# Kernel optimization log

Hardware: AMD Instinct MI355X
Metric: run time of the kernel (lower is better)

## Reference

```python
import jax, jax.numpy as jnp
import numpy as np

IN_CHANNELS = 8
CHANNELS = 8
MASK_OUT_STRIDE = 4
N_IMGS, H, W = 2, 128, 192
N_INST = 256
WEIGHT_NUMS = [(IN_CHANNELS + 2) * CHANNELS, CHANNELS * CHANNELS, CHANNELS * 1]  # [80, 64, 8]
BIAS_NUMS = [CHANNELS, CHANNELS, 1]
NUM_GEN_PARAMS = sum(WEIGHT_NUMS) + sum(BIAS_NUMS)  # 169


def setup_inputs() -> dict:
    key = jax.random.key(0)
    k1, k2, k3, k4, k5 = jax.random.split(key, 5)
    mask_feats = jax.random.normal(k1, (N_IMGS, IN_CHANNELS, H, W), dtype=jnp.float32)
    mask_head_params = jax.random.normal(k2, (N_INST, NUM_GEN_PARAMS), dtype=jnp.float32) * 0.1
    # instance center locations in image coordinates (stride-8 map covers 1024x1536 px)
    instance_locations = jax.random.uniform(k3, (N_INST, 2), dtype=jnp.float32) * jnp.array([W * 8.0, H * 8.0])
    soi = jnp.array([64.0, 128.0, 256.0, 512.0, 1024.0], dtype=jnp.float32)
    im_inds = jax.random.randint(k4, (N_INST,), 0, N_IMGS, dtype=jnp.int32)
    fpn_levels = jax.random.randint(k5, (N_INST,), 0, 5, dtype=jnp.int32)
    return {
        "mask_feats": mask_feats,
        "mask_head_params": mask_head_params,
        "instance_locations": instance_locations,
        "soi": soi,
        "im_inds": im_inds,
        "fpn_levels": fpn_levels,
        "mask_feat_stride": 8,
    }


def compute_locations(h, w, stride):
    shifts_x = jnp.arange(w, dtype=jnp.float32) * stride + stride // 2
    shifts_y = jnp.arange(h, dtype=jnp.float32) * stride + stride // 2
    ys, xs = jnp.meshgrid(shifts_y, shifts_x, indexing="ij")
    return jnp.stack([xs.ravel(), ys.ravel()], axis=1)  # [H*W, 2] (x, y)


def _interp_axis(x, size_in, factor, axis):
    # align_corners=True resize from (size_in+1) samples to (size_in*factor+1):
    # src coordinate of output i is exactly i / factor.
    idx = jnp.arange(size_in * factor + 1)
    i0 = idx // factor
    frac = ((idx % factor).astype(x.dtype)) / factor
    a = jnp.take(x, i0, axis=axis)
    b = jnp.take(x, jnp.minimum(i0 + 1, size_in), axis=axis)
    shape = [1] * x.ndim
    shape[axis] = -1
    f = frac.reshape(shape)
    return a * (1 - f) + b * f


def aligned_bilinear(t, factor):
    # Faithful to AdelaiDet aligned_bilinear: replicate-pad (0,1,0,1), bilinear
    # align_corners=True to (h*f+1, w*f+1), replicate-pad (f//2, 0) top/left, crop.
    if factor == 1:
        return t
    n, c, h, w = t.shape
    t = jnp.pad(t, ((0, 0), (0, 0), (0, 1), (0, 1)), mode="edge")
    t = _interp_axis(t, h, factor, 2)
    t = _interp_axis(t, w, factor, 3)
    p = factor // 2
    t = jnp.pad(t, ((0, 0), (0, 0), (p, 0), (p, 0)), mode="edge")
    return t[:, :, : h * factor, : w * factor]


def reference(mask_feats, mask_head_params, instance_locations, soi, im_inds, fpn_levels, mask_feat_stride):
    n_inst = mask_head_params.shape[0]
    _, c_in, h, w = mask_feats.shape
    hw = h * w

    # relative coordinates, normalized by size-of-interest per FPN level
    locations = compute_locations(h, w, mask_feat_stride)  # [HW, 2]
    rel = instance_locations[:, None, :] - locations[None, :, :]  # [n, HW, 2]
    rel = jnp.transpose(rel, (0, 2, 1))  # [n, 2, HW]
    rel = rel / soi[fpn_levels][:, None, None]
    rel = rel.astype(mask_feats.dtype)

    feats = mask_feats[im_inds].reshape(n_inst, c_in, hw)  # [n, C, HW]
    x = jnp.concatenate([rel, feats], axis=1)  # [n, C+2, HW]

    # parse dynamic params
    splits = np.cumsum(WEIGHT_NUMS + BIAS_NUMS)[:-1]
    w0, w1, w2, b0, b1, b2 = jnp.split(mask_head_params, splits, axis=1)
    w0 = w0.reshape(n_inst, CHANNELS, c_in + 2)
    w1 = w1.reshape(n_inst, CHANNELS, CHANNELS)
    w2 = w2.reshape(n_inst, 1, CHANNELS)

    # grouped 1x1 conv stack == per-instance batched matmul + bias (+ReLU)
    x = jax.nn.relu(jnp.einsum("noi,nip->nop", w0, x) + b0[:, :, None])
    x = jax.nn.relu(jnp.einsum("noi,nip->nop", w1, x) + b1[:, :, None])
    x = jnp.einsum("noi,nip->nop", w2, x) + b2[:, :, None]  # [n, 1, HW]

    logits = x.reshape(n_inst, 1, h, w)
    factor = mask_feat_stride // MASK_OUT_STRIDE
    return aligned_bilinear(logits, factor)  # [n, 1, h*factor, w*factor]
```

## Files before the change

### kernel.cpp

```cpp
#include <hip/hip_runtime.h>


#define HI 128
#define WI 192
#define HW_ (HI * WI)
#define NP 169
#define NOUT_W 384
#define NOUT_H 256

typedef float v2f __attribute__((ext_vector_type(2)));

__device__ __forceinline__ v2f splat(float x) { v2f r; r.x = x; r.y = x; return r; }
__device__ __forceinline__ v2f vfma(v2f a, v2f b, v2f c) {
    return __builtin_elementwise_fma(a, b, c);
}
__device__ __forceinline__ v2f vrelu(v2f a) {
    return __builtin_elementwise_max(a, splat(0.0f));
}

__global__ __launch_bounds__(512, 4) void dynmask_kernel(
    const float* __restrict__ feats,
    const float* __restrict__ params,
    const float* __restrict__ locs,
    const float* __restrict__ soi,
    const int*   __restrict__ im_inds,
    const int*   __restrict__ lvls,
    float*       __restrict__ out)
{
    __shared__ __align__(16) float L[65 * WI];

    const int b  = blockIdx.x;
    const int n  = b >> 1;
    const int hh = b & 1;
    const int t  = threadIdx.x;
    const int R0 = hh ? 63 : 0;

    const int   im    = im_inds[n];
    const float s     = soi[lvls[n]];
    const float inv_s = 1.0f / s;
    const float ixv   = locs[2 * n + 0];
    const float iyv   = locs[2 * n + 1];
    const float* __restrict__ P = params + n * NP;
    const float* __restrict__ F = feats + im * (8 * HW_);

    const float step = 8.0f * inv_s;
    const float ax   = (ixv - 4.0f) * inv_s;
    const float ay   = (iyv - 4.0f) * inv_s;

    for (int idx = t; idx < 3120; idx += 512) {
        const int p   = R0 * WI + (idx << 2);
        const int py  = p / WI;
        const int px0 = p - py * WI;
        const float ry  = ay - (float)py * step;
        const float rx0 = ax - (float)px0 * step;
        v2f rxp[2];
        rxp[0].x = rx0;                rxp[0].y = rx0 - step;
        rxp[1].x = rx0 - 2.0f * step;  rxp[1].y = rx0 - 3.0f * step;

        v2f fv[8][2];
        #pragma unroll
        for (int k = 0; k < 8; ++k) {
            const float4 v = *reinterpret_cast<const float4*>(F + k * HW_ + p);
            fv[k][0].x = v.x; fv[k][0].y = v.y;
            fv[k][1].x = v.z; fv[k][1].y = v.w;
        }

        v2f h0[8][2];
        #pragma unroll
        for (int o = 0; o < 8; ++o) {
            const float base = fmaf(P[o * 10 + 1], ry, P[152 + o]);
            const v2f   bv   = splat(base);
            const v2f   wx   = splat(P[o * 10 + 0]);
            h0[o][0] = vfma(wx, rxp[0], bv);
            h0[o][1] = vfma(wx, rxp[1], bv);
            #pragma unroll
            for (int k = 0; k < 8; ++k) {
                const v2f w = splat(P[o * 10 + 2 + k]);
                h0[o][0] = vfma(w, fv[k][0], h0[o][0]);
                h0[o][1] = vfma(w, fv[k][1], h0[o][1]);
            }
            h0[o][0] = vrelu(h0[o][0]);
            h0[o][1] = vrelu(h0[o][1]);
        }

        v2f h1[8][2];
        #pragma unroll
        for (int o = 0; o < 8; ++o) {
            const v2f bb = splat(P[160 + o]);
            h1[o][0] = bb;
            h1[o][1] = bb;
            #pragma unroll
            for (int i = 0; i < 8; ++i) {
                const v2f w = splat(P[80 + o * 8 + i]);
                h1[o][0] = vfma(w, h0[i][0], h1[o][0]);
                h1[o][1] = vfma(w, h0[i][1], h1[o][1]);
            }
            h1[o][0] = vrelu(h1[o][0]);
            h1[o][1] = vrelu(h1[o][1]);
        }

        v2f lg[2];
        lg[0] = splat(P[168]);
        lg[1] = lg[0];
        #pragma unroll
        for (int i = 0; i < 8; ++i) {
            const v2f w = splat(P[144 + i]);
            lg[0] = vfma(w, h1[i][0], lg[0]);
            lg[1] = vfma(w, h1[i][1], lg[1]);
        }

        float4 st;
        st.x = lg[0].x; st.y = lg[0].y; st.z = lg[1].x; st.w = lg[1].y;
        *reinterpret_cast<float4*>(&L[idx << 2]) = st;
    }

    __syncthreads();

    const int Y0 = hh << 7;
    float* __restrict__ O = out + n * (NOUT_H * NOUT_W) + Y0 * NOUT_W;
    for (int g = t; g < 6144; g += 512) {
        const int yq = g / 48;
        const int c  = g - yq * 48;
        const int y  = Y0 + yq;
        const int iy2 = (y == 0) ? 0 : (y - 1);
        const int ry0 = iy2 >> 1;
        const int fy  = iy2 & 1;
        const int lr0 = ry0 - R0;
        const int j0  = c << 2;
        const int jm  = (c == 0) ? 0 : (j0 - 1);

        const float* row0 = &L[lr0 * WI];
        float4 v  = *reinterpret_cast<const float4*>(row0 + j0);
        float  vm = row0[jm];
        if (fy) {
            const int lr1 = min(ry0 + 1, 127) - R0;
            const float* row1 = &L[lr1 * WI];
            const float4 w  = *reinterpret_cast<const float4*>(row1 + j0);
            const float  wm = row1[jm];
            v.x = 0.5f * (v.x + w.x); v.y = 0.5f * (v.y + w.y);
            v.z = 0.5f * (v.z + w.z); v.w = 0.5f * (v.w + w.w);
            vm  = 0.5f * (vm + wm);
        }
        float4 r0, r1;
        r0.x = 0.5f * (vm + v.x);  r0.y = v.x;
        r0.z = 0.5f * (v.x + v.y); r0.w = v.y;
        r1.x = 0.5f * (v.y + v.z); r1.y = v.z;
        r1.z = 0.5f * (v.z + v.w); r1.w = v.w;

        float* o8 = O + (g << 3);
        *reinterpret_cast<float4*>(o8)     = r0;
        *reinterpret_cast<float4*>(o8 + 4) = r1;
    }
}

extern "C" void kernel_launch(void* const* d_in, const int* in_sizes, int n_in,
                              void* d_out, int out_size, void* d_ws, size_t ws_size,
                              hipStream_t stream) {
    const float* feats   = (const float*)d_in[0];
    const float* params  = (const float*)d_in[1];
    const float* locs    = (const float*)d_in[2];
    const float* soi     = (const float*)d_in[3];
    const int*   im_inds = (const int*)d_in[4];
    const int*   lvls    = (const int*)d_in[5];
    float*       out     = (float*)d_out;
    dynmask_kernel<<<512, 512, 0, stream>>>(feats, params, locs, soi, im_inds, lvls, out);
}
```

Baseline: 149.9 us.

## Split each instance into four row quarters and halve per-thread pixel work

Each instance is now handled by four blocks covering 32 (+1 halo) logit rows instead of two blocks of 64, which doubles the grid and halves the shared-memory tile. Each thread computes 2 pixels instead of 4 with 8-byte loads, and launch bounds now request 8 blocks per CU, aiming for lower register pressure and higher occupancy. The trade-off is more redundant halo-row MLP work, narrower global loads, and more per-block parameter loads.

```diff
diff --git a/kernel.cpp b/kernel.cpp
--- a/kernel.cpp
+++ b/kernel.cpp
@@ -18,7 +18,7 @@
     return __builtin_elementwise_max(a, splat(0.0f));
 }
 
-__global__ __launch_bounds__(512, 4) void dynmask_kernel(
+__global__ __launch_bounds__(512, 8) void dynmask_kernel(
     const float* __restrict__ feats,
     const float* __restrict__ params,
     const float* __restrict__ locs,
@@ -27,13 +27,13 @@
     const int*   __restrict__ lvls,
     float*       __restrict__ out)
 {
-    __shared__ __align__(16) float L[65 * WI];
+    __shared__ __align__(16) float L[33 * WI];
 
     const int b  = blockIdx.x;
-    const int n  = b >> 1;
-    const int hh = b & 1;
+    const int n  = b >> 2;
+    const int qq = b & 3;
     const int t  = threadIdx.x;
-    const int R0 = hh ? 63 : 0;
+    const int R0 = (qq == 0) ? 0 : (32 * qq - 1);
 
     const int   im    = im_inds[n];
     const float s     = soi[lvls[n]];
@@ -47,78 +47,56 @@
     const float ax   = (ixv - 4.0f) * inv_s;
     const float ay   = (iyv - 4.0f) * inv_s;
 
-    for (int idx = t; idx < 3120; idx += 512) {
-        const int p   = R0 * WI + (idx << 2);
-        const int py  = p / WI;
-        const int px0 = p - py * WI;
+    for (int idx = t; idx < 3168; idx += 512) {
+        const int r   = idx / 96;
+        const int c2  = idx - r * 96;
+        const int py  = R0 + r;
+        const int px0 = c2 * 2;
+        const int gp  = py * WI + px0;
+
         const float ry  = ay - (float)py * step;
         const float rx0 = ax - (float)px0 * step;
-        v2f rxp[2];
-        rxp[0].x = rx0;                rxp[0].y = rx0 - step;
-        rxp[1].x = rx0 - 2.0f * step;  rxp[1].y = rx0 - 3.0f * step;
+        v2f rx; rx.x = rx0; rx.y = rx0 - step;
 
-        v2f fv[8][2];
+        v2f fv[8];
         #pragma unroll
-        for (int k = 0; k < 8; ++k) {
-            const float4 v = *reinterpret_cast<const float4*>(F + k * HW_ + p);
-            fv[k][0].x = v.x; fv[k][0].y = v.y;
-            fv[k][1].x = v.z; fv[k][1].y = v.w;
-        }
+        for (int k = 0; k < 8; ++k)
+            fv[k] = *reinterpret_cast<const v2f*>(F + k * HW_ + gp);
 
-        v2f h0[8][2];
+        v2f h0[8];
         #pragma unroll
         for (int o = 0; o < 8; ++o) {
             const float base = fmaf(P[o * 10 + 1], ry, P[152 + o]);
-            const v2f   bv   = splat(base);
-            const v2f   wx   = splat(P[o * 10 + 0]);
-            h0[o][0] = vfma(wx, rxp[0], bv);
-            h0[o][1] = vfma(wx, rxp[1], bv);
+            h0[o] = vfma(splat(P[o * 10 + 0]), rx, splat(base));
             #pragma unroll
-            for (int k = 0; k < 8; ++k) {
-                const v2f w = splat(P[o * 10 + 2 + k]);
-                h0[o][0] = vfma(w, fv[k][0], h0[o][0]);
-                h0[o][1] = vfma(w, fv[k][1], h0[o][1]);
-            }
-            h0[o][0] = vrelu(h0[o][0]);
-            h0[o][1] = vrelu(h0[o][1]);
+            for (int k = 0; k < 8; ++k)
+                h0[o] = vfma(splat(P[o * 10 + 2 + k]), fv[k], h0[o]);
+            h0[o] = vrelu(h0[o]);
         }
 
-        v2f h1[8][2];
+        v2f h1[8];
         #pragma unroll
         for (int o = 0; o < 8; ++o) {
-            const v2f bb = splat(P[160 + o]);
-            h1[o][0] = bb;
-            h1[o][1] = bb;
+            h1[o] = splat(P[160 + o]);
             #pragma unroll
-            for (int i = 0; i < 8; ++i) {
-                const v2f w = splat(P[80 + o * 8 + i]);
-                h1[o][0] = vfma(w, h0[i][0], h1[o][0]);
-                h1[o][1] = vfma(w, h0[i][1], h1[o][1]);
-            }
-            h1[o][0] = vrelu(h1[o][0]);
-            h1[o][1] = vrelu(h1[o][1]);
+            for (int i = 0; i < 8; ++i)
+                h1[o] = vfma(splat(P[80 + o * 8 + i]), h0[i], h1[o]);
+            h1[o] = vrelu(h1[o]);
         }
 
-        v2f lg[2];
-        lg[0] = splat(P[168]);
-        lg[1] = lg[0];
+        v2f lg = splat(P[168]);
         #pragma unroll
-        for (int i = 0; i < 8; ++i) {
-            const v2f w = splat(P[144 + i]);
-            lg[0] = vfma(w, h1[i][0], lg[0]);
-            lg[1] = vfma(w, h1[i][1], lg[1]);
-        }
+        for (int i = 0; i < 8; ++i)
+            lg = vfma(splat(P[144 + i]), h1[i], lg);
 
-        float4 st;
-        st.x = lg[0].x; st.y = lg[0].y; st.z = lg[1].x; st.w = lg[1].y;
-        *reinterpret_cast<float4*>(&L[idx << 2]) = st;
+        *reinterpret_cast<v2f*>(&L[idx * 2]) = lg;
     }
 
     __syncthreads();
 
-    const int Y0 = hh << 7;
+    const int Y0 = qq << 6;
     float* __restrict__ O = out + n * (NOUT_H * NOUT_W) + Y0 * NOUT_W;
-    for (int g = t; g < 6144; g += 512) {
+    for (int g = t; g < 3072; g += 512) {
         const int yq = g / 48;
         const int c  = g - yq * 48;
         const int y  = Y0 + yq;
@@ -133,7 +111,7 @@
         float4 v  = *reinterpret_cast<const float4*>(row0 + j0);
         float  vm = row0[jm];
         if (fy) {
-            const int lr1 = min(ry0 + 1, 127) - R0;
+            const int lr1 = min(ry0 + 1, HI - 1) - R0;
             const float* row1 = &L[lr1 * WI];
             const float4 w  = *reinterpret_cast<const float4*>(row1 + j0);
             const float  wm = row1[jm];
@@ -163,5 +141,5 @@
     const int*   im_inds = (const int*)d_in[4];
     const int*   lvls    = (const int*)d_in[5];
     float*       out     = (float*)d_out;
-    dynmask_kernel<<<512, 512, 0, stream>>>(feats, params, locs, soi, im_inds, lvls, out);
+    dynmask_kernel<<<1024, 512, 0, stream>>>(feats, params, locs, soi, im_inds, lvls, out);
 }
```

Result: slower. 184.9 us (+23.3%).
